# Kernel optimization log

Measured on AMD Instinct MI355X. Metric: run time of the kernel, lower is better.

## Reference

```python
import jax, jax.numpy as jnp
import numpy as np

N_NODES = 100000
N_EDGES = 3200000


def gcn_conv(x, W, b, src, dst, n_nodes):
    # x: [N, Fin] -> [N, Fout]; PyG GCNConv: linear, add self-loops,
    # symmetric norm D^-1/2 A_hat D^-1/2, sum-aggregate over incoming edges, + bias
    h = x @ W  # [N, Fout]
    loop = jnp.arange(n_nodes, dtype=src.dtype)
    src2 = jnp.concatenate([src, loop])
    dst2 = jnp.concatenate([dst, loop])
    deg = jax.ops.segment_sum(jnp.ones_like(dst2, dtype=h.dtype), dst2, num_segments=n_nodes)
    dinv = jnp.where(deg > 0, jax.lax.rsqrt(deg), 0.0)
    norm = dinv[src2] * dinv[dst2]  # [E+N]
    msgs = h[src2] * norm[:, None]  # gather + scale
    out = jax.ops.segment_sum(msgs, dst2, num_segments=n_nodes)  # scatter-add
    return out + b


def setup_inputs() -> dict:
    key = jax.random.key(0)
    k1, k2, k3, k4 = jax.random.split(key, 4)
    x = jax.random.normal(k1, (N_NODES, 16), dtype=jnp.float32)
    edge_index = jax.random.randint(k2, (2, N_EDGES), 0, N_NODES, dtype=jnp.int64)
    W1 = jax.random.normal(k3, (16, 32), dtype=jnp.float32) * (1.0 / np.sqrt(16))
    b1 = jnp.zeros((32,), dtype=jnp.float32)
    W2 = jax.random.normal(k4, (32, 3), dtype=jnp.float32) * (1.0 / np.sqrt(32))
    b2 = jnp.zeros((3,), dtype=jnp.float32)
    return {"x": x, "edge_index": edge_index, "W1": W1, "b1": b1, "W2": W2, "b2": b2}


def reference(x, edge_index, W1, b1, W2, b2):
    src, dst = edge_index[0], edge_index[1]
    n = x.shape[0]
    h = gcn_conv(x, W1, b1, src, dst, n)
    h = jax.nn.relu(h)
    h = gcn_conv(h, W2, b2, src, dst, n)
    return jax.nn.log_softmax(h, axis=1)
```

## Files before the change

### kernel.cpp

```cpp
#include <hip/hip_runtime.h>
#include <math.h>


#define NN 100000
#define NE 3200000
#define BSH 7
#define NPB 128
#define NB  ((NN + NPB - 1) / NPB)
#define EPB 12544
#define CAP 6144
#define SCAP 5632

__device__ __forceinline__ float bl(unsigned u) { return __uint_as_float(u << 16); }
__device__ __forceinline__ float bh(unsigned u) { return __uint_as_float(u & 0xFFFF0000u); }
__device__ __forceinline__ unsigned rne(float f) {
    unsigned u = __float_as_uint(f);
    return (u + 0x7FFFu + ((u >> 16) & 1u)) >> 16;
}

typedef int vint4 __attribute__((ext_vector_type(4)));


__global__ void __launch_bounds__(256) k_zero(int* __restrict__ bcur) {
    int t = blockIdx.x * 256 + threadIdx.x;
    if (t < NB) bcur[t] = 0;
}

__global__ void __launch_bounds__(1024) k_partition(
        const int* __restrict__ src, const int* __restrict__ dst,
        int* __restrict__ bcur, unsigned int* __restrict__ ebuf, int E) {
    __shared__ int hist[NB];
    __shared__ int lbase[NB];
    __shared__ int gbase[NB];
    __shared__ int lcur[NB];
    __shared__ unsigned int sebuf[EPB];
    __shared__ unsigned short sbkt[EPB];
    __shared__ int wsum[16];
    int tid = threadIdx.x;
    int e0 = blockIdx.x * EPB;
    int e1 = min(e0 + EPB, E);
    int cnt = e1 - e0;
    int cnt4 = cnt >> 2;
    if (tid < NB) { hist[tid] = 0; lcur[tid] = 0; }
    __syncthreads();
    const vint4* d4 = (const vint4*)(dst + e0);
    vint4 dc[4];
#pragma unroll
    for (int r = 0; r < 4; r++) {
        int i4 = r * 1024 + tid;
        if (i4 < cnt4) {
            dc[r] = d4[i4];
            atomicAdd(&hist[dc[r].x >> BSH], 1);
            atomicAdd(&hist[dc[r].y >> BSH], 1);
            atomicAdd(&hist[dc[r].z >> BSH], 1);
            atomicAdd(&hist[dc[r].w >> BSH], 1);
        }
    }
    __syncthreads();
    int lane = tid & 63, w = tid >> 6;
    {
        int v = (tid < NB) ? hist[tid] : 0;
        int incl = v;
#pragma unroll
        for (int off = 1; off < 64; off <<= 1) {
            int u = __shfl_up(incl, off);
            if (lane >= off) incl += u;
        }
        if (lane == 63) wsum[w] = incl;
        __syncthreads();
        int woff = 0;
#pragma unroll
        for (int k = 0; k < 16; k++) woff += (k < w) ? wsum[k] : 0;
        int excl = incl - v + woff;
        if (tid < NB) {
            lbase[tid] = excl;
            gbase[tid] = tid * CAP + (v ? atomicAdd(&bcur[tid], v) : 0);
        }
        __syncthreads();
    }
    const vint4* s4 = (const vint4*)(src + e0);
#pragma unroll
    for (int r = 0; r < 4; r++) {
        int i4 = r * 1024 + tid;
        if (i4 < cnt4) {
            vint4 sv = s4[i4];
            int d, b, p;
            d = dc[r].x; b = d >> BSH; p = lbase[b] + atomicAdd(&lcur[b], 1);
            sebuf[p] = (unsigned)sv.x | ((unsigned)(d & (NPB - 1)) << 20);
            sbkt[p] = (unsigned short)b;
            d = dc[r].y; b = d >> BSH; p = lbase[b] + atomicAdd(&lcur[b], 1);
            sebuf[p] = (unsigned)sv.y | ((unsigned)(d & (NPB - 1)) << 20);
            sbkt[p] = (unsigned short)b;
            d = dc[r].z; b = d >> BSH; p = lbase[b] + atomicAdd(&lcur[b], 1);
            sebuf[p] = (unsigned)sv.z | ((unsigned)(d & (NPB - 1)) << 20);
            sbkt[p] = (unsigned short)b;
            d = dc[r].w; b = d >> BSH; p = lbase[b] + atomicAdd(&lcur[b], 1);
            sebuf[p] = (unsigned)sv.w | ((unsigned)(d & (NPB - 1)) << 20);
            sbkt[p] = (unsigned short)b;
        }
    }
    __syncthreads();
    for (int p = tid; p < cnt; p += 1024) {
        int b = sbkt[p];
        ebuf[gbase[b] + (p - lbase[b])] = sebuf[p];
    }
}

__global__ void __launch_bounds__(256) k_B(
        const unsigned int* __restrict__ ebuf, const int* __restrict__ bcur,
        const float* __restrict__ x, int* __restrict__ deg,
        unsigned int* __restrict__ xsb, int N) {
    __shared__ int hist[NPB];
    int b = blockIdx.x, tid = threadIdx.x;
    int beg = b * CAP, cnt = bcur[b];
    int cnt4 = cnt >> 2;
    if (tid < NPB) hist[tid] = 0;
    __syncthreads();
    const uint4* e4 = (const uint4*)(ebuf + beg);
    for (int j4 = tid; j4 < cnt4; j4 += 256) {
        uint4 pv = e4[j4];
        atomicAdd(&hist[pv.x >> 20], 1);
        atomicAdd(&hist[pv.y >> 20], 1);
        atomicAdd(&hist[pv.z >> 20], 1);
        atomicAdd(&hist[pv.w >> 20], 1);
    }
    for (int j = (cnt4 << 2) + tid; j < cnt; j += 256)
        atomicAdd(&hist[ebuf[beg + j] >> 20], 1);
    __syncthreads();
    if (tid < NPB) {
        int node = b * NPB + tid;
        if (node < N) {
            int v = hist[tid];
            deg[node] = v;
            float di = rsqrtf((float)(v + 1));
            const float4* x4 = (const float4*)(x + (size_t)node * 16);
            float4 A = x4[0], Bv = x4[1], Cv = x4[2], Dv = x4[3];
            uint4 o0, o1;
            o0.x = rne(A.x * di) | (rne(A.y * di) << 16);
            o0.y = rne(A.z * di) | (rne(A.w * di) << 16);
            o0.z = rne(Bv.x * di) | (rne(Bv.y * di) << 16);
            o0.w = rne(Bv.z * di) | (rne(Bv.w * di) << 16);
            o1.x = rne(Cv.x * di) | (rne(Cv.y * di) << 16);
            o1.y = rne(Cv.z * di) | (rne(Cv.w * di) << 16);
            o1.z = rne(Dv.x * di) | (rne(Dv.y * di) << 16);
            o1.w = rne(Dv.z * di) | (rne(Dv.w * di) << 16);
            uint4* op = (uint4*)xsb;
            op[(size_t)node * 2 + 0] = o0;
            op[(size_t)node * 2 + 1] = o1;
        }
    }
}

__global__ void __launch_bounds__(512) k_L1(
        const unsigned int* __restrict__ ebuf, const int* __restrict__ bcur,
        const int* __restrict__ deg, const unsigned int* __restrict__ xsb,
        const float* __restrict__ W1, const float* __restrict__ b1,
        const float* __restrict__ W2, unsigned int* __restrict__ g2b, int N) {
    __shared__ int scol[SCAP];
    __shared__ float sacc[NPB][17];
    __shared__ int sdeg[NPB];
    __shared__ int base[NPB];
    __shared__ int lcur[NPB];
    __shared__ float sdinv[NPB];
    __shared__ float W1s[512];
    __shared__ float W2s[96];
    __shared__ float b1s[32];
    __shared__ int wsum[2];
    int b = blockIdx.x, tid = threadIdx.x;
    int beg = b * CAP;
    int cnt = bcur[b];
    int cl = min(cnt, SCAP);
    int cl4 = cl >> 2;
    W1s[tid] = W1[tid];
    if (tid < 96) W2s[tid] = W2[tid];
    if (tid < 32) b1s[tid] = b1[tid];
    int lane = tid & 63, w = tid >> 6;
    int v = 0;
    if (tid < NPB) {
        int node = b * NPB + tid;
        v = (node < N) ? deg[node] : 0;
        sdeg[tid] = v;
        lcur[tid] = 0;
        sdinv[tid] = rsqrtf((float)(v + 1));
    }
    int incl = v;
#pragma unroll
    for (int off = 1; off < 64; off <<= 1) {
        int u = __shfl_up(incl, off);
        if (lane >= off) incl += u;
    }
    if (tid < NPB && lane == 63) wsum[w] = incl;
    __syncthreads();
    if (tid < NPB) base[tid] = incl - v + ((w == 1) ? wsum[0] : 0);
    __syncthreads();
    const uint4* e4 = (const uint4*)(ebuf + beg);
    for (int j4 = tid; j4 < cl4; j4 += 512) {
        uint4 pv = e4[j4];
        int dl, pos;
        dl = (int)(pv.x >> 20); pos = base[dl] + atomicAdd(&lcur[dl], 1);
        if (pos < SCAP) scol[pos] = (int)(pv.x & 0xFFFFF);
        dl = (int)(pv.y >> 20); pos = base[dl] + atomicAdd(&lcur[dl], 1);
        if (pos < SCAP) scol[pos] = (int)(pv.y & 0xFFFFF);
        dl = (int)(pv.z >> 20); pos = base[dl] + atomicAdd(&lcur[dl], 1);
        if (pos < SCAP) scol[pos] = (int)(pv.z & 0xFFFFF);
        dl = (int)(pv.w >> 20); pos = base[dl] + atomicAdd(&lcur[dl], 1);
        if (pos < SCAP) scol[pos] = (int)(pv.w & 0xFFFFF);
    }
    for (int j = (cl4 << 2) + tid; j < cl; j += 512) {
        unsigned pe = ebuf[beg + j];
        int dl = (int)(pe >> 20);
        int pos = base[dl] + atomicAdd(&lcur[dl], 1);
        if (pos < SCAP) scol[pos] = (int)(pe & 0xFFFFF);
    }
    __syncthreads();
    {
        int g = tid >> 4;
        int lq = tid & 15;
        int r = lq >> 1, c = lq & 1;
        const uint4* xb = (const uint4*)xsb;
#pragma unroll
        for (int p = 0; p < 4; p++) {
            int nib = p * 32 + g;
            int jb = base[nib];
            int je = jb + sdeg[nib];
            float a0 = 0.f, a1 = 0.f, a2 = 0.f, a3 = 0.f;
            float a4 = 0.f, a5 = 0.f, a6 = 0.f, a7 = 0.f;
            int j = jb + r;
            while (j + 8 < je) {
                int s0 = scol[j], s1 = scol[j + 8];
                uint4 q0 = xb[(size_t)s0 * 2 + c];
                uint4 q1 = xb[(size_t)s1 * 2 + c];
                a0 += bl(q0.x); a1 += bh(q0.x); a2 += bl(q0.y); a3 += bh(q0.y);
                a4 += bl(q0.z); a5 += bh(q0.z); a6 += bl(q0.w); a7 += bh(q0.w);
                a0 += bl(q1.x); a1 += bh(q1.x); a2 += bl(q1.y); a3 += bh(q1.y);
                a4 += bl(q1.z); a5 += bh(q1.z); a6 += bl(q1.w); a7 += bh(q1.w);
                j += 16;
            }
            if (j < je) {
                int s = scol[j];
                uint4 qq = xb[(size_t)s * 2 + c];
                a0 += bl(qq.x); a1 += bh(qq.x); a2 += bl(qq.y); a3 += bh(qq.y);
                a4 += bl(qq.z); a5 += bh(qq.z); a6 += bl(qq.w); a7 += bh(qq.w);
            }
#pragma unroll
            for (int off = 8; off >= 2; off >>= 1) {
                a0 += __shfl_down(a0, off);
                a1 += __shfl_down(a1, off);
                a2 += __shfl_down(a2, off);
                a3 += __shfl_down(a3, off);
                a4 += __shfl_down(a4, off);
                a5 += __shfl_down(a5, off);
                a6 += __shfl_down(a6, off);
                a7 += __shfl_down(a7, off);
            }
            if (lq < 2) {
                sacc[nib][c * 8 + 0] = a0; sacc[nib][c * 8 + 1] = a1;
                sacc[nib][c * 8 + 2] = a2; sacc[nib][c * 8 + 3] = a3;
                sacc[nib][c * 8 + 4] = a4; sacc[nib][c * 8 + 5] = a5;
                sacc[nib][c * 8 + 6] = a6; sacc[nib][c * 8 + 7] = a7;
            }
        }
    }
    __syncthreads();
    if (tid < NPB) {
        int node = b * NPB + tid;
        if (node < N) {
            float di = sdinv[tid];
            const uint4* xb = (const uint4*)xsb;
            uint4 s0 = xb[(size_t)node * 2], s1 = xb[(size_t)node * 2 + 1];
            float a[16] = {
                sacc[tid][0] + bl(s0.x),  sacc[tid][1] + bh(s0.x),
                sacc[tid][2] + bl(s0.y),  sacc[tid][3] + bh(s0.y),
                sacc[tid][4] + bl(s0.z),  sacc[tid][5] + bh(s0.z),
                sacc[tid][6] + bl(s0.w),  sacc[tid][7] + bh(s0.w),
                sacc[tid][8] + bl(s1.x),  sacc[tid][9] + bh(s1.x),
                sacc[tid][10] + bl(s1.y), sacc[tid][11] + bh(s1.y),
                sacc[tid][12] + bl(s1.z), sacc[tid][13] + bh(s1.z),
                sacc[tid][14] + bl(s1.w), sacc[tid][15] + bh(s1.w)};
            float p0 = 0.f, p1 = 0.f, p2 = 0.f;
#pragma unroll
            for (int jj = 0; jj < 32; jj++) {
                float o = 0.f;
#pragma unroll
                for (int k = 0; k < 16; k++) o = fmaf(a[k], W1s[k * 32 + jj], o);
                float z = fmaxf(fmaf(di, o, b1s[jj]), 0.f);
                p0 = fmaf(z, W2s[jj * 3 + 0], p0);
                p1 = fmaf(z, W2s[jj * 3 + 1], p1);
                p2 = fmaf(z, W2s[jj * 3 + 2], p2);
            }
            uint2 o;
            o.x = rne(p0 * di) | (rne(p1 * di) << 16);
            o.y = rne(p2 * di);
            ((uint2*)g2b)[node] = o;
        }
    }
}

__global__ void __launch_bounds__(512) k_L2(
        const unsigned int* __restrict__ ebuf, const int* __restrict__ bcur,
        const int* __restrict__ deg, const unsigned int* __restrict__ g2b,
        const float* __restrict__ b2, float* __restrict__ out, int N) {
    __shared__ int scol[SCAP];
    __shared__ int sdeg[NPB];
    __shared__ int base[NPB];
    __shared__ int lcur[NPB];
    __shared__ float sdinv[NPB];
    __shared__ int wsum[2];
    int b = blockIdx.x, tid = threadIdx.x;
    int beg = b * CAP;
    int cnt = bcur[b];
    int cl = min(cnt, SCAP);
    int cl4 = cl >> 2;
    int lane = tid & 63, w = tid >> 6;
    int v = 0;
    if (tid < NPB) {
        int node = b * NPB + tid;
        v = (node < N) ? deg[node] : 0;
        sdeg[tid] = v;
        lcur[tid] = 0;
        sdinv[tid] = rsqrtf((float)(v + 1));
    }
    int incl = v;
#pragma unroll
    for (int off = 1; off < 64; off <<= 1) {
        int u = __shfl_up(incl, off);
        if (lane >= off) incl += u;
    }
    if (tid < NPB && lane == 63) wsum[w] = incl;
    __syncthreads();
    if (tid < NPB) base[tid] = incl - v + ((w == 1) ? wsum[0] : 0);
    __syncthreads();
    const uint4* e4 = (const uint4*)(ebuf + beg);
    for (int j4 = tid; j4 < cl4; j4 += 512) {
        uint4 pv = e4[j4];
        int dl, pos;
        dl = (int)(pv.x >> 20); pos = base[dl] + atomicAdd(&lcur[dl], 1);
        if (pos < SCAP) scol[pos] = (int)(pv.x & 0xFFFFF);
        dl = (int)(pv.y >> 20); pos = base[dl] + atomicAdd(&lcur[dl], 1);
        if (pos < SCAP) scol[pos] = (int)(pv.y & 0xFFFFF);
        dl = (int)(pv.z >> 20); pos = base[dl] + atomicAdd(&lcur[dl], 1);
        if (pos < SCAP) scol[pos] = (int)(pv.z & 0xFFFFF);
        dl = (int)(pv.w >> 20); pos = base[dl] + atomicAdd(&lcur[dl], 1);
        if (pos < SCAP) scol[pos] = (int)(pv.w & 0xFFFFF);
    }
    for (int j = (cl4 << 2) + tid; j < cl; j += 512) {
        unsigned pe = ebuf[beg + j];
        int dl = (int)(pe >> 20);
        int pos = base[dl] + atomicAdd(&lcur[dl], 1);
        if (pos < SCAP) scol[pos] = (int)(pe & 0xFFFFF);
    }
    __syncthreads();
    {
        int lo = tid & 7;
        const uint2* gb = (const uint2*)g2b;
#pragma unroll
        for (int p = 0; p < 2; p++) {
            int nib = p * 64 + (tid >> 3);
            int node = b * NPB + nib;
            int jb = base[nib];
            int je = jb + sdeg[nib];
            float a0 = 0.f, a1 = 0.f, a2 = 0.f;
            int j = jb + lo;
            while (j + 8 < je) {
                uint2 v0 = gb[scol[j]];
                uint2 v1 = gb[scol[j + 8]];
                a0 += bl(v0.x); a1 += bh(v0.x); a2 += bl(v0.y);
                a0 += bl(v1.x); a1 += bh(v1.x); a2 += bl(v1.y);
                j += 16;
            }
            if (j < je) {
                uint2 vv = gb[scol[j]];
                a0 += bl(vv.x); a1 += bh(vv.x); a2 += bl(vv.y);
            }
#pragma unroll
            for (int off = 4; off >= 1; off >>= 1) {
                a0 += __shfl_down(a0, off);
                a1 += __shfl_down(a1, off);
                a2 += __shfl_down(a2, off);
            }
            if (lo == 0 && node < N) {
                float di = sdinv[nib];
                uint2 sv = gb[node];
                float v0 = fmaf(di, a0 + bl(sv.x), b2[0]);
                float v1 = fmaf(di, a1 + bh(sv.x), b2[1]);
                float v2 = fmaf(di, a2 + bl(sv.y), b2[2]);
                float m = fmaxf(v0, fmaxf(v1, v2));
                float lse = m + logf(expf(v0 - m) + expf(v1 - m) + expf(v2 - m));
                out[(size_t)node * 3 + 0] = v0 - lse;
                out[(size_t)node * 3 + 1] = v1 - lse;
                out[(size_t)node * 3 + 2] = v2 - lse;
            }
        }
    }
}


extern "C" void kernel_launch(void* const* d_in, const int* in_sizes, int n_in,
                              void* d_out, int out_size, void* d_ws, size_t ws_size,
                              hipStream_t stream) {
    const float* x  = (const float*)d_in[0];
    const int*   ei = (const int*)d_in[1];
    const float* W1 = (const float*)d_in[2];
    const float* b1 = (const float*)d_in[3];
    const float* W2 = (const float*)d_in[4];
    const float* b2 = (const float*)d_in[5];
    float* out = (float*)d_out;

    const int* src = ei;
    const int* dst = ei + NE;

    unsigned int* ebuf = (unsigned int*)d_ws;
    unsigned int* xsb  = ebuf + (size_t)NB * CAP;
    unsigned int* g2b  = xsb + (size_t)NN * 8;
    int*          deg  = (int*)(g2b + (size_t)NN * 2);
    int*          bcur = deg + NN;

    const int B = 256;
    int gbP = (NE + EPB - 1) / EPB;
    int gbZ = (NB + B - 1) / B;

    k_zero<<<gbZ, B, 0, stream>>>(bcur);
    k_partition<<<gbP, 1024, 0, stream>>>(src, dst, bcur, ebuf, NE);
    k_B<<<NB, B, 0, stream>>>(ebuf, bcur, x, deg, xsb, NN);
    k_L1<<<NB, 512, 0, stream>>>(ebuf, bcur, deg, xsb, W1, b1, W2, g2b, NN);
    k_L2<<<NB, 512, 0, stream>>>(ebuf, bcur, deg, g2b, b2, out, NN);
}
```

Baseline: 82.61 us.

## Split bf16 node features into two half-planes and gather each separately

Stores the 16-feature bf16 rows as two separate planes of 8 features (16 bytes each) instead of interleaved 32-byte rows. The layer-1 gather then processes each plane in its own pass, with all 16 lanes striding over edges, and reduces across 16 lanes. The idea is to shrink each plane's footprint so it stays better in cache and to make each random gather touch a 16-byte segment. The cost is two passes over the edge list, a deeper shuffle reduction, and two reads per neighbor spread across separate cache lines.

```diff
diff --git a/kernel.cpp b/kernel.cpp
--- a/kernel.cpp
+++ b/kernel.cpp
@@ -144,9 +144,10 @@
             o1.y = rne(Cv.z * di) | (rne(Cv.w * di) << 16);
             o1.z = rne(Dv.x * di) | (rne(Dv.y * di) << 16);
             o1.w = rne(Dv.z * di) | (rne(Dv.w * di) << 16);
-            uint4* op = (uint4*)xsb;
-            op[(size_t)node * 2 + 0] = o0;
-            op[(size_t)node * 2 + 1] = o1;
+            uint4* op0 = (uint4*)xsb;
+            uint4* op1 = op0 + NN;
+            op0[node] = o0;
+            op1[node] = o1;
         }
     }
 }
@@ -216,48 +217,52 @@
     {
         int g = tid >> 4;
         int lq = tid & 15;
-        int r = lq >> 1, c = lq & 1;
-        const uint4* xb = (const uint4*)xsb;
-#pragma unroll
-        for (int p = 0; p < 4; p++) {
-            int nib = p * 32 + g;
-            int jb = base[nib];
-            int je = jb + sdeg[nib];
-            float a0 = 0.f, a1 = 0.f, a2 = 0.f, a3 = 0.f;
-            float a4 = 0.f, a5 = 0.f, a6 = 0.f, a7 = 0.f;
-            int j = jb + r;
-            while (j + 8 < je) {
-                int s0 = scol[j], s1 = scol[j + 8];
-                uint4 q0 = xb[(size_t)s0 * 2 + c];
-                uint4 q1 = xb[(size_t)s1 * 2 + c];
-                a0 += bl(q0.x); a1 += bh(q0.x); a2 += bl(q0.y); a3 += bh(q0.y);
-                a4 += bl(q0.z); a5 += bh(q0.z); a6 += bl(q0.w); a7 += bh(q0.w);
-                a0 += bl(q1.x); a1 += bh(q1.x); a2 += bl(q1.y); a3 += bh(q1.y);
-                a4 += bl(q1.z); a5 += bh(q1.z); a6 += bl(q1.w); a7 += bh(q1.w);
-                j += 16;
-            }
-            if (j < je) {
-                int s = scol[j];
-                uint4 qq = xb[(size_t)s * 2 + c];
-                a0 += bl(qq.x); a1 += bh(qq.x); a2 += bl(qq.y); a3 += bh(qq.y);
-                a4 += bl(qq.z); a5 += bh(qq.z); a6 += bl(qq.w); a7 += bh(qq.w);
-            }
-#pragma unroll
-            for (int off = 8; off >= 2; off >>= 1) {
-                a0 += __shfl_down(a0, off);
-                a1 += __shfl_down(a1, off);
-                a2 += __shfl_down(a2, off);
-                a3 += __shfl_down(a3, off);
-                a4 += __shfl_down(a4, off);
-                a5 += __shfl_down(a5, off);
-                a6 += __shfl_down(a6, off);
-                a7 += __shfl_down(a7, off);
-            }
-            if (lq < 2) {
-                sacc[nib][c * 8 + 0] = a0; sacc[nib][c * 8 + 1] = a1;
-                sacc[nib][c * 8 + 2] = a2; sacc[nib][c * 8 + 3] = a3;
-                sacc[nib][c * 8 + 4] = a4; sacc[nib][c * 8 + 5] = a5;
-                sacc[nib][c * 8 + 6] = a6; sacc[nib][c * 8 + 7] = a7;
+        const uint4* xb0 = (const uint4*)xsb;
+        const uint4* xb1 = xb0 + NN;
+#pragma unroll
+        for (int c = 0; c < 2; c++) {
+            const uint4* xbc = c ? xb1 : xb0;
+#pragma unroll
+            for (int p = 0; p < 4; p++) {
+                int nib = p * 32 + g;
+                int jb = base[nib];
+                int je = jb + sdeg[nib];
+                float a0 = 0.f, a1 = 0.f, a2 = 0.f, a3 = 0.f;
+                float a4 = 0.f, a5 = 0.f, a6 = 0.f, a7 = 0.f;
+                int j = jb + lq;
+                while (j + 16 < je) {
+                    int s0 = scol[j], s1 = scol[j + 16];
+                    uint4 q0 = xbc[s0];
+                    uint4 q1 = xbc[s1];
+                    a0 += bl(q0.x); a1 += bh(q0.x); a2 += bl(q0.y); a3 += bh(q0.y);
+                    a4 += bl(q0.z); a5 += bh(q0.z); a6 += bl(q0.w); a7 += bh(q0.w);
+                    a0 += bl(q1.x); a1 += bh(q1.x); a2 += bl(q1.y); a3 += bh(q1.y);
+                    a4 += bl(q1.z); a5 += bh(q1.z); a6 += bl(q1.w); a7 += bh(q1.w);
+                    j += 32;
+                }
+                if (j < je) {
+                    int s = scol[j];
+                    uint4 qq = xbc[s];
+                    a0 += bl(qq.x); a1 += bh(qq.x); a2 += bl(qq.y); a3 += bh(qq.y);
+                    a4 += bl(qq.z); a5 += bh(qq.z); a6 += bl(qq.w); a7 += bh(qq.w);
+                }
+#pragma unroll
+                for (int off = 8; off >= 1; off >>= 1) {
+                    a0 += __shfl_down(a0, off);
+                    a1 += __shfl_down(a1, off);
+                    a2 += __shfl_down(a2, off);
+                    a3 += __shfl_down(a3, off);
+                    a4 += __shfl_down(a4, off);
+                    a5 += __shfl_down(a5, off);
+                    a6 += __shfl_down(a6, off);
+                    a7 += __shfl_down(a7, off);
+                }
+                if (lq == 0) {
+                    sacc[nib][c * 8 + 0] = a0; sacc[nib][c * 8 + 1] = a1;
+                    sacc[nib][c * 8 + 2] = a2; sacc[nib][c * 8 + 3] = a3;
+                    sacc[nib][c * 8 + 4] = a4; sacc[nib][c * 8 + 5] = a5;
+                    sacc[nib][c * 8 + 6] = a6; sacc[nib][c * 8 + 7] = a7;
+                }
             }
         }
     }
@@ -266,8 +271,9 @@
         int node = b * NPB + tid;
         if (node < N) {
             float di = sdinv[tid];
-            const uint4* xb = (const uint4*)xsb;
-            uint4 s0 = xb[(size_t)node * 2], s1 = xb[(size_t)node * 2 + 1];
+            const uint4* xb0 = (const uint4*)xsb;
+            const uint4* xb1 = xb0 + NN;
+            uint4 s0 = xb0[node], s1 = xb1[node];
             float a[16] = {
                 sacc[tid][0] + bl(s0.x),  sacc[tid][1] + bh(s0.x),
                 sacc[tid][2] + bl(s0.y),  sacc[tid][3] + bh(s0.y),
```

After: 97.71 us. 1.18x slower.
